# Kernel tuning notes

Hardware: AMD Instinct MI355X
Metric: run time of the kernel (lower is better)

The kernel has to match this reference:

```python
import jax, jax.numpy as jnp
import numpy as np
import math

SCALE = math.sqrt(256.0)

def setup_inputs() -> dict:
    key = jax.random.key(0)
    k1, k2, k3, k4, k5 = jax.random.split(key, 5)
    B, C, T, D = 8, 80, 2048, 256
    bound = 1.0 / math.sqrt(C)
    x = jax.random.normal(k1, (B, C, T), dtype=jnp.float32)
    Wk = jax.random.uniform(k2, (D, C), minval=-bound, maxval=bound, dtype=jnp.float32)
    bk = jax.random.uniform(k3, (D,), minval=-bound, maxval=bound, dtype=jnp.float32)
    Wq = jax.random.uniform(k4, (D, C), minval=-bound, maxval=bound, dtype=jnp.float32)
    bq = jax.random.uniform(k5, (D,), minval=-bound, maxval=bound, dtype=jnp.float32)
    return {"x": x, "Wk": Wk, "bk": bk, "Wq": Wq, "bq": bq}

def reference(x, Wk, bk, Wq, bq):
    # x: [B, C=80, T]; work in time-major layout [B, T, C]
    xt = jnp.swapaxes(x, 1, 2)                      # [B, T, C]
    K = xt @ Wk.T + bk                              # [B, T, 256]
    Q = xt @ Wq.T + bq                              # [B, T, 256]
    # softmax over last dim (dim=2 in torch) of K Q^T / sqrt(256)
    att = jax.nn.softmax(jnp.einsum('bid,bjd->bij', K, Q) / SCALE, axis=2)
    # original per-timestep loop is exactly att @ xt (values = raw input, no V proj)
    out = jnp.einsum('bij,bjc->bic', att, xt)       # [B, T, C]
    return jnp.swapaxes(out, 1, 2)                  # [B, C, T]
```

## Files before the change

### kernel.cpp

```cpp
#include <hip/hip_runtime.h>
#include <hip/hip_bf16.h>
#include <math.h>

typedef __bf16 bf16;
typedef __bf16 bf16x8 __attribute__((ext_vector_type(8)));
typedef float  f32x4  __attribute__((ext_vector_type(4)));
typedef float  f32x16 __attribute__((ext_vector_type(16)));
typedef uint32_t u32x4 __attribute__((ext_vector_type(4)));

#define MFMA16(a, b, c) __builtin_amdgcn_mfma_f32_16x16x32_bf16((a), (b), (c), 0, 0, 0)
#define MFMA32(a, b, c) __builtin_amdgcn_mfma_f32_32x32x16_bf16((a), (b), (c), 0, 0, 0)

typedef const uint32_t __attribute__((address_space(1)))* gq_t;
typedef uint32_t __attribute__((address_space(3)))* lq_t;

constexpr int B_ = 8, C_ = 80, T_ = 2048, D_ = 256;
constexpr int NS = 4;
constexpr float LOG2E_16 = 0.090169989f;

static __device__ inline uint32_t pkbf(float lo, float hi) {
  bf16 l = (bf16)lo, h = (bf16)hi;
  uint16_t lb = __builtin_bit_cast(uint16_t, l), hb = __builtin_bit_cast(uint16_t, h);
  return (uint32_t)lb | ((uint32_t)hb << 16);
}

__global__ __launch_bounds__(256) void proj_kernel(
    const float* __restrict__ x,
    const float* __restrict__ Wk,
    const float* __restrict__ bk,
    const float* __restrict__ Wq,
    const float* __restrict__ bq,
    bf16* __restrict__ Kb,
    bf16* __restrict__ Qb,
    bf16* __restrict__ xbf)
{
  const int t0   = blockIdx.x * 32;
  const int b    = blockIdx.y;
  const int tid  = threadIdx.x;
  const int w    = tid >> 6;
  const int lane = tid & 63;
  const int h    = lane >> 4;
  const int lr   = lane & 15;

  const float* xb = x + (size_t)b * C_ * T_;

  {
    bf16* ob = xbf + (size_t)b * C_ * T_;
    auto conv8 = [&](int c, int ch) {
      const f32x4* sp = reinterpret_cast<const f32x4*>(xb + (size_t)c * T_ + t0 + ch * 8);
      f32x4 v0 = sp[0], v1 = sp[1];
      bf16x8 o;
      #pragma unroll
      for (int e = 0; e < 4; ++e) { o[e] = (bf16)v0[e]; o[e + 4] = (bf16)v1[e]; }
      *reinterpret_cast<bf16x8*>(ob + (size_t)c * T_ + t0 + ch * 8) = o;
    };
    conv8(tid >> 2, tid & 3);
    if (tid < 64) conv8(64 + (tid >> 2), tid & 3);
  }

  bf16x8 afrag[2][3];
  #pragma unroll
  for (int ib = 0; ib < 2; ++ib) {
    int t = t0 + ib * 16 + lr;
    #pragma unroll
    for (int ks = 0; ks < 3; ++ks) {
      bf16x8 v;
      #pragma unroll
      for (int e = 0; e < 8; ++e) {
        int c = ks * 32 + h * 8 + e;
        float val;
        if (c < 80)       val = xb[c * T_ + t];
        else if (c == 80) val = 1.0f;
        else              val = 0.0f;
        v[e] = (bf16)val;
      }
      afrag[ib][ks] = v;
    }
  }

  const int nb0 = w * 4;
  #pragma unroll
  for (int mat = 0; mat < 2; ++mat) {
    const float* W    = mat ? Wq : Wk;
    const float* bias = mat ? bq : bk;
    bf16* outp        = mat ? Qb : Kb;

    f32x4 acc[2][4];
    #pragma unroll
    for (int ib = 0; ib < 2; ++ib)
      #pragma unroll
      for (int nb = 0; nb < 4; ++nb)
        acc[ib][nb] = f32x4{0.f, 0.f, 0.f, 0.f};

    #pragma unroll
    for (int nb = 0; nb < 4; ++nb) {
      int d = (nb0 + nb) * 16 + lr;
      #pragma unroll
      for (int ks = 0; ks < 3; ++ks) {
        bf16x8 bv;
        #pragma unroll
        for (int e = 0; e < 8; ++e) {
          int c = ks * 32 + h * 8 + e;
          float val;
          if (c < 80)       val = W[d * C_ + c];
          else if (c == 80) val = bias[d];
          else              val = 0.0f;
          bv[e] = (bf16)val;
        }
        #pragma unroll
        for (int ib = 0; ib < 2; ++ib)
          acc[ib][nb] = MFMA16(afrag[ib][ks], bv, acc[ib][nb]);
      }
    }

    #pragma unroll
    for (int ib = 0; ib < 2; ++ib)
      #pragma unroll
      for (int nb = 0; nb < 4; ++nb) {
        int d = (nb0 + nb) * 16 + lr;
        #pragma unroll
        for (int r = 0; r < 4; ++r) {
          int t = t0 + ib * 16 + h * 4 + r;
          outp[(size_t)(b * T_ + t) * D_ + d] = (bf16)acc[ib][nb][r];
        }
      }
  }
}

__global__ __launch_bounds__(256, 2) void attn_kernel(
    const bf16* __restrict__ Kb,
    const bf16* __restrict__ Qb,
    const bf16* __restrict__ xbf,
    float* __restrict__ Opart,
    float* __restrict__ mpart,
    float* __restrict__ lpart)
{
  constexpr int BN = 32, NT = T_ / BN;
  constexpr int JT_PER = NT / NS;
  __shared__ bf16 qlds[2][BN * D_];

  const int flat = blockIdx.x;
  const int b    = flat & 7;
  const int rem  = flat >> 3;
  const int it   = rem & 15;
  const int s    = rem >> 4;
  const int i0   = it * 128;

  const int tid  = threadIdx.x;
  const int w    = tid >> 6;
  const int lane = tid & 63;
  const int il   = lane & 31;
  const int hi   = lane >> 5;
  const int iw   = i0 + w * 32;

  const bf16* Kbase = Kb  + (size_t)b * T_ * D_;
  const bf16* Qbase = Qb  + (size_t)b * T_ * D_;
  const bf16* Vbase = xbf + (size_t)b * C_ * T_;

  bf16x8 kf[16];
  {
    const bf16* kp = Kbase + (size_t)(iw + il) * D_ + hi * 8;
    #pragma unroll
    for (int ks = 0; ks < 16; ++ks)
      kf[ks] = *reinterpret_cast<const bf16x8*>(kp + ks * 16);
  }

  f32x16 oacc[3];
  #pragma unroll
  for (int cb = 0; cb < 3; ++cb)
    #pragma unroll
    for (int r = 0; r < 16; ++r) oacc[cb][r] = 0.f;
  float m_run = -INFINITY, l_run = 0.f;

  auto stage = [&](int jt, int buf) {
    #pragma unroll
    for (int q = 0; q < 4; ++q) {
      int f = tid + 256 * q;
      int j = f >> 5, c = f & 31;
      const bf16* src = Qbase + (size_t)(jt * BN + j) * D_ + ((c ^ j) << 3);
      __builtin_amdgcn_global_load_lds((gq_t)src,
          (lq_t)&qlds[buf][(q * 256 + w * 64) * 8], 16, 0, 0);
    }
  };

  const int jt0 = s * JT_PER, jtend = jt0 + JT_PER;

  stage(jt0, 0);
  asm volatile("s_waitcnt vmcnt(0)" ::: "memory");
  __syncthreads();

  int cur = 0;
  for (int jt = jt0; jt < jtend; ++jt, cur ^= 1) {
    if (jt + 1 < jtend) stage(jt + 1, cur ^ 1);

    bf16x8 vf[3][2];
    #pragma unroll
    for (int cb = 0; cb < 3; ++cb)
      #pragma unroll
      for (int kj = 0; kj < 2; ++kj)
        vf[cb][kj] = *reinterpret_cast<const bf16x8*>(
            Vbase + (size_t)(cb * 32 + il) * T_ + jt * BN + hi * 8 + kj * 16);

    f32x16 s0, s1;
    #pragma unroll
    for (int r = 0; r < 16; ++r) { s0[r] = 0.f; s1[r] = 0.f; }
    __builtin_amdgcn_s_setprio(1);
    #pragma unroll
    for (int ks = 0; ks < 16; ks += 2) {
      bf16x8 qa0 = *reinterpret_cast<const bf16x8*>(
          &qlds[cur][il * 256 + (((hi + 2 * ks) ^ il) << 3)]);
      bf16x8 qa1 = *reinterpret_cast<const bf16x8*>(
          &qlds[cur][il * 256 + (((hi + 2 * (ks + 1)) ^ il) << 3)]);
      s0 = MFMA32(qa0, kf[ks], s0);
      s1 = MFMA32(qa1, kf[ks + 1], s1);
    }
    __builtin_amdgcn_s_setprio(0);
    f32x16 sacc = s0 + s1;

    float p16[16];
    #pragma unroll
    for (int r = 0; r < 16; ++r) p16[r] = sacc[r];
    float mx01 = fmaxf(p16[0], p16[1]);
    float mx23 = fmaxf(p16[2], p16[3]);
    float mx45 = fmaxf(p16[4], p16[5]);
    float mx67 = fmaxf(p16[6], p16[7]);
    float mx89 = fmaxf(p16[8], p16[9]);
    float mxab = fmaxf(p16[10], p16[11]);
    float mxcd = fmaxf(p16[12], p16[13]);
    float mxef = fmaxf(p16[14], p16[15]);
    float mx = fmaxf(fmaxf(fmaxf(mx01, mx23), fmaxf(mx45, mx67)),
                     fmaxf(fmaxf(mx89, mxab), fmaxf(mxcd, mxef)));
    mx = fmaxf(mx, __shfl_xor(mx, 32));

    if (!__all(mx <= m_run + 48.f)) {
      float mnew  = fmaxf(m_run, mx);
      float alpha = exp2f((m_run - mnew) * LOG2E_16);
      m_run = mnew;
      l_run *= alpha;
      #pragma unroll
      for (int cb = 0; cb < 3; ++cb)
        #pragma unroll
        for (int r = 0; r < 16; ++r) oacc[cb][r] *= alpha;
    }
    float rs = 0.f;
    #pragma unroll
    for (int r = 0; r < 16; ++r) {
      p16[r] = exp2f((p16[r] - m_run) * LOG2E_16);
      rs += p16[r];
    }
    rs += __shfl_xor(rs, 32);
    l_run += rs;

    uint32_t a0 = pkbf(p16[0],  p16[1]),  a1 = pkbf(p16[2],  p16[3]);
    uint32_t c0 = pkbf(p16[4],  p16[5]),  c1 = pkbf(p16[6],  p16[7]);
    uint32_t a2 = pkbf(p16[8],  p16[9]),  a3 = pkbf(p16[10], p16[11]);
    uint32_t c2 = pkbf(p16[12], p16[13]), c3 = pkbf(p16[14], p16[15]);
    uint32_t a0s = __shfl_xor(a0, 32), a1s = __shfl_xor(a1, 32);
    uint32_t c0s = __shfl_xor(c0, 32), c1s = __shfl_xor(c1, 32);
    uint32_t a2s = __shfl_xor(a2, 32), a3s = __shfl_xor(a3, 32);
    uint32_t c2s = __shfl_xor(c2, 32), c3s = __shfl_xor(c3, 32);
    const bool hh = (hi != 0);
    u32x4 pb0 = { hh ? c0s : a0, hh ? c1s : a1, hh ? c0 : a0s, hh ? c1 : a1s };
    u32x4 pb1 = { hh ? c2s : a2, hh ? c3s : a3, hh ? c2 : a2s, hh ? c3 : a3s };
    bf16x8 pbf0 = __builtin_bit_cast(bf16x8, pb0);
    bf16x8 pbf1 = __builtin_bit_cast(bf16x8, pb1);

    __builtin_amdgcn_s_setprio(1);
    #pragma unroll
    for (int cb = 0; cb < 3; ++cb) {
      oacc[cb] = MFMA32(vf[cb][0], pbf0, oacc[cb]);
      oacc[cb] = MFMA32(vf[cb][1], pbf1, oacc[cb]);
    }
    __builtin_amdgcn_s_setprio(0);

    asm volatile("s_waitcnt vmcnt(0)" ::: "memory");
    __syncthreads();
  }

  float* ob = Opart + (size_t)(s * B_ + b) * C_ * T_;
  #pragma unroll
  for (int cb = 0; cb < 3; ++cb)
    #pragma unroll
    for (int r = 0; r < 16; ++r) {
      if (cb < 2 || r < 8) {
        int c = cb * 32 + (r & 3) + 8 * (r >> 2) + 4 * hi;
        ob[(size_t)c * T_ + iw + il] = oacc[cb][r];
      }
    }
  if (lane < 32) {
    mpart[(size_t)(s * B_ + b) * T_ + iw + il] = m_run;
    lpart[(size_t)(s * B_ + b) * T_ + iw + il] = l_run;
  }
}

__global__ __launch_bounds__(256) void merge_kernel(
    const float* __restrict__ Opart,
    const float* __restrict__ mpart,
    const float* __restrict__ lpart,
    float* __restrict__ out)
{
  const int b      = blockIdx.y;
  const int tid    = threadIdx.x;
  const int slot   = tid & 15;
  const int cstrip = tid >> 4;
  const int t4     = blockIdx.x * 64 + slot * 4;

  f32x4 m[NS], e[NS];
  f32x4 mmax;
  #pragma unroll
  for (int s2 = 0; s2 < NS; ++s2)
    m[s2] = *reinterpret_cast<const f32x4*>(&mpart[(size_t)(s2 * B_ + b) * T_ + t4]);
  #pragma unroll
  for (int r = 0; r < 4; ++r) {
    mmax[r] = m[0][r];
    #pragma unroll
    for (int s2 = 1; s2 < NS; ++s2) mmax[r] = fmaxf(mmax[r], m[s2][r]);
  }
  f32x4 lsum = f32x4{0.f, 0.f, 0.f, 0.f};
  #pragma unroll
  for (int s2 = 0; s2 < NS; ++s2) {
    f32x4 lv = *reinterpret_cast<const f32x4*>(&lpart[(size_t)(s2 * B_ + b) * T_ + t4]);
    #pragma unroll
    for (int r = 0; r < 4; ++r) e[s2][r] = exp2f((m[s2][r] - mmax[r]) * LOG2E_16);
    lsum += e[s2] * lv;
  }
  f32x4 inv;
  #pragma unroll
  for (int r = 0; r < 4; ++r) inv[r] = 1.0f / lsum[r];

  #pragma unroll
  for (int cc = 0; cc < 5; ++cc) {
    const int c = cstrip * 5 + cc;
    f32x4 acc = f32x4{0.f, 0.f, 0.f, 0.f};
    #pragma unroll
    for (int s2 = 0; s2 < NS; ++s2)
      acc += *reinterpret_cast<const f32x4*>(
                 &Opart[((size_t)(s2 * B_ + b) * C_ + c) * T_ + t4]) * e[s2];
    *reinterpret_cast<f32x4*>(&out[((size_t)b * C_ + c) * T_ + t4]) = acc * inv;
  }
}

extern "C" void kernel_launch(void* const* d_in, const int* in_sizes, int n_in,
                              void* d_out, int out_size, void* d_ws, size_t ws_size,
                              hipStream_t stream) {
  (void)in_sizes; (void)n_in; (void)out_size; (void)ws_size;
  const float* x  = (const float*)d_in[0];
  const float* Wk = (const float*)d_in[1];
  const float* bk = (const float*)d_in[2];
  const float* Wq = (const float*)d_in[3];
  const float* bq = (const float*)d_in[4];
  float* out = (float*)d_out;

  char* ws = (char*)d_ws;
  const size_t MB = 1024 * 1024;
  bf16*  Kb    = (bf16*)(ws);
  bf16*  Qb    = (bf16*)(ws + 8 * MB);
  bf16*  xbf   = (bf16*)(ws + 16 * MB);
  float* Opart = (float*)(ws + 19 * MB);
  float* mpart = (float*)(ws + 41 * MB);
  float* lpart = (float*)(ws + 42 * MB);

  dim3 blk(256);
  dim3 g1(T_ / 32, B_);
  proj_kernel<<<g1, blk, 0, stream>>>(x, Wk, bk, Wq, bq, Kb, Qb, xbf);
  attn_kernel<<<dim3(16 * NS * B_), blk, 0, stream>>>(Kb, Qb, xbf, Opart, mpart, lpart);
  dim3 g3(T_ / 64, B_);
  merge_kernel<<<g3, blk, 0, stream>>>(Opart, mpart, lpart, out);
}
```

Baseline: 70.63 us.

## Pre-tile V into MFMA fragment order and stage it through LDS

```diff
diff --git a/kernel.cpp b/kernel.cpp
--- a/kernel.cpp
+++ b/kernel.cpp
@@ -23,6 +23,8 @@
   uint16_t lb = __builtin_bit_cast(uint16_t, l), hb = __builtin_bit_cast(uint16_t, h);
   return (uint32_t)lb | ((uint32_t)hb << 16);
 }
+
+constexpr int VF_TILE = 3 * 2 * 2 * 32 * 8;
 
 __global__ __launch_bounds__(256) void proj_kernel(
     const float* __restrict__ x,
@@ -32,7 +34,7 @@
     const float* __restrict__ bq,
     bf16* __restrict__ Kb,
     bf16* __restrict__ Qb,
-    bf16* __restrict__ xbf)
+    bf16* __restrict__ Vf)
 {
   const int t0   = blockIdx.x * 32;
   const int b    = blockIdx.y;
@@ -45,17 +47,27 @@
   const float* xb = x + (size_t)b * C_ * T_;
 
   {
-    bf16* ob = xbf + (size_t)b * C_ * T_;
-    auto conv8 = [&](int c, int ch) {
-      const f32x4* sp = reinterpret_cast<const f32x4*>(xb + (size_t)c * T_ + t0 + ch * 8);
-      f32x4 v0 = sp[0], v1 = sp[1];
-      bf16x8 o;
-      #pragma unroll
-      for (int e = 0; e < 4; ++e) { o[e] = (bf16)v0[e]; o[e + 4] = (bf16)v1[e]; }
-      *reinterpret_cast<bf16x8*>(ob + (size_t)c * T_ + t0 + ch * 8) = o;
-    };
-    conv8(tid >> 2, tid & 3);
-    if (tid < 64) conv8(64 + (tid >> 2), tid & 3);
+    bf16* vout = Vf + (size_t)(b * 64 + blockIdx.x) * VF_TILE;
+    #pragma unroll
+    for (int g = 0; g < 2; ++g) {
+      int f = tid + g * 256;
+      if (f < 384) {
+        int il2 = f & 31, hi2 = (f >> 5) & 1, kj2 = (f >> 6) & 1, cb2 = f >> 7;
+        int c = cb2 * 32 + il2;
+        bf16x8 o;
+        if (c < 80) {
+          const float* sp = xb + (size_t)c * T_ + t0 + kj2 * 16 + hi2 * 8;
+          f32x4 v0 = *reinterpret_cast<const f32x4*>(sp);
+          f32x4 v1 = *reinterpret_cast<const f32x4*>(sp + 4);
+          #pragma unroll
+          for (int e = 0; e < 4; ++e) { o[e] = (bf16)v0[e]; o[e + 4] = (bf16)v1[e]; }
+        } else {
+          #pragma unroll
+          for (int e = 0; e < 8; ++e) o[e] = (bf16)0.f;
+        }
+        *reinterpret_cast<bf16x8*>(vout + f * 8) = o;
+      }
+    }
   }
 
   bf16x8 afrag[2][3];
@@ -130,7 +142,7 @@
 __global__ __launch_bounds__(256, 2) void attn_kernel(
     const bf16* __restrict__ Kb,
     const bf16* __restrict__ Qb,
-    const bf16* __restrict__ xbf,
+    const bf16* __restrict__ Vf,
     float* __restrict__ Opart,
     float* __restrict__ mpart,
     float* __restrict__ lpart)
@@ -138,6 +150,7 @@
   constexpr int BN = 32, NT = T_ / BN;
   constexpr int JT_PER = NT / NS;
   __shared__ bf16 qlds[2][BN * D_];
+  __shared__ bf16 vlds[2][VF_TILE];
 
   const int flat = blockIdx.x;
   const int b    = flat & 7;
@@ -153,9 +166,9 @@
   const int hi   = lane >> 5;
   const int iw   = i0 + w * 32;
 
-  const bf16* Kbase = Kb  + (size_t)b * T_ * D_;
-  const bf16* Qbase = Qb  + (size_t)b * T_ * D_;
-  const bf16* Vbase = xbf + (size_t)b * C_ * T_;
+  const bf16* Kbase = Kb + (size_t)b * T_ * D_;
+  const bf16* Qbase = Qb + (size_t)b * T_ * D_;
+  const bf16* Vbase = Vf + (size_t)b * 64 * VF_TILE;
 
   bf16x8 kf[16];
   {
@@ -181,6 +194,12 @@
       __builtin_amdgcn_global_load_lds((gq_t)src,
           (lq_t)&qlds[buf][(q * 256 + w * 64) * 8], 16, 0, 0);
     }
+    const bf16* vsrc = Vbase + (size_t)jt * VF_TILE;
+    __builtin_amdgcn_global_load_lds((gq_t)(vsrc + (size_t)tid * 8),
+        (lq_t)&vlds[buf][(w * 64) * 8], 16, 0, 0);
+    if (w < 2)
+      __builtin_amdgcn_global_load_lds((gq_t)(vsrc + (size_t)(256 + tid) * 8),
+          (lq_t)&vlds[buf][(256 + w * 64) * 8], 16, 0, 0);
   };
 
   const int jt0 = s * JT_PER, jtend = jt0 + JT_PER;
@@ -199,35 +218,27 @@
       #pragma unroll
       for (int kj = 0; kj < 2; ++kj)
         vf[cb][kj] = *reinterpret_cast<const bf16x8*>(
-            Vbase + (size_t)(cb * 32 + il) * T_ + jt * BN + hi * 8 + kj * 16);
-
-    f32x16 s0, s1;
-    #pragma unroll
-    for (int r = 0; r < 16; ++r) { s0[r] = 0.f; s1[r] = 0.f; }
+            &vlds[cur][(size_t)(((cb * 2 + kj) * 2 + hi) * 32 + il) * 8]);
+
+    f32x16 sacc;
+    #pragma unroll
+    for (int r = 0; r < 16; ++r) sacc[r] = 0.f;
     __builtin_amdgcn_s_setprio(1);
     #pragma unroll
-    for (int ks = 0; ks < 16; ks += 2) {
-      bf16x8 qa0 = *reinterpret_cast<const bf16x8*>(
+    for (int ks = 0; ks < 16; ++ks) {
+      bf16x8 qa = *reinterpret_cast<const bf16x8*>(
           &qlds[cur][il * 256 + (((hi + 2 * ks) ^ il) << 3)]);
-      bf16x8 qa1 = *reinterpret_cast<const bf16x8*>(
-          &qlds[cur][il * 256 + (((hi + 2 * (ks + 1)) ^ il) << 3)]);
-      s0 = MFMA32(qa0, kf[ks], s0);
-      s1 = MFMA32(qa1, kf[ks + 1], s1);
+      sacc = MFMA32(qa, kf[ks], sacc);
     }
     __builtin_amdgcn_s_setprio(0);
-    f32x16 sacc = s0 + s1;
 
     float p16[16];
     #pragma unroll
     for (int r = 0; r < 16; ++r) p16[r] = sacc[r];
-    float mx01 = fmaxf(p16[0], p16[1]);
-    float mx23 = fmaxf(p16[2], p16[3]);
-    float mx45 = fmaxf(p16[4], p16[5]);
-    float mx67 = fmaxf(p16[6], p16[7]);
-    float mx89 = fmaxf(p16[8], p16[9]);
-    float mxab = fmaxf(p16[10], p16[11]);
-    float mxcd = fmaxf(p16[12], p16[13]);
-    float mxef = fmaxf(p16[14], p16[15]);
+    float mx01 = fmaxf(p16[0], p16[1]),  mx23 = fmaxf(p16[2], p16[3]);
+    float mx45 = fmaxf(p16[4], p16[5]),  mx67 = fmaxf(p16[6], p16[7]);
+    float mx89 = fmaxf(p16[8], p16[9]),  mxab = fmaxf(p16[10], p16[11]);
+    float mxcd = fmaxf(p16[12], p16[13]), mxef = fmaxf(p16[14], p16[15]);
     float mx = fmaxf(fmaxf(fmaxf(mx01, mx23), fmaxf(mx45, mx67)),
                      fmaxf(fmaxf(mx89, mxab), fmaxf(mxcd, mxef)));
     mx = fmaxf(mx, __shfl_xor(mx, 32));
@@ -248,7 +259,6 @@
       p16[r] = exp2f((p16[r] - m_run) * LOG2E_16);
       rs += p16[r];
     }
-    rs += __shfl_xor(rs, 32);
     l_run += rs;
 
     uint32_t a0 = pkbf(p16[0],  p16[1]),  a1 = pkbf(p16[2],  p16[3]);
@@ -277,6 +287,8 @@
     __syncthreads();
   }
 
+  l_run += __shfl_xor(l_run, 32);
+
   float* ob = Opart + (size_t)(s * B_ + b) * C_ * T_;
   #pragma unroll
   for (int cb = 0; cb < 3; ++cb)
@@ -355,15 +367,15 @@
   const size_t MB = 1024 * 1024;
   bf16*  Kb    = (bf16*)(ws);
   bf16*  Qb    = (bf16*)(ws + 8 * MB);
-  bf16*  xbf   = (bf16*)(ws + 16 * MB);
+  bf16*  Vf    = (bf16*)(ws + 16 * MB);
   float* Opart = (float*)(ws + 19 * MB);
   float* mpart = (float*)(ws + 41 * MB);
   float* lpart = (float*)(ws + 42 * MB);
 
   dim3 blk(256);
   dim3 g1(T_ / 32, B_);
-  proj_kernel<<<g1, blk, 0, stream>>>(x, Wk, bk, Wq, bq, Kb, Qb, xbf);
-  attn_kernel<<<dim3(16 * NS * B_), blk, 0, stream>>>(Kb, Qb, xbf, Opart, mpart, lpart);
+  proj_kernel<<<g1, blk, 0, stream>>>(x, Wk, bk, Wq, bq, Kb, Qb, Vf);
+  attn_kernel<<<dim3(16 * NS * B_), blk, 0, stream>>>(Kb, Qb, Vf, Opart, mpart, lpart);
   dim3 g3(T_ / 64, B_);
   merge_kernel<<<g3, blk, 0, stream>>>(Opart, mpart, lpart, out);
 }
```

New measurement: 69.40 us. About the same (-1.7%).
